# Kernel tuning notes

Hardware: AMD Instinct MI355X
Metric: run time of the kernel (lower is better)

The kernel has to match this reference:

```python
import jax, jax.numpy as jnp
import numpy as np

B, D, H, K, P = 16384, 64, 256, 8, 3  # batch, lattice dim, hidden, expressivity, num_pars


def setup_inputs() -> dict:
    key = jax.random.key(0)
    k0, k1, k2 = jax.random.split(key, 3)
    # U(1) angles in [0, 2*pi)
    z = jax.random.uniform(k0, (B, D), dtype=jnp.float32) * (2.0 * jnp.pi)
    # per-step conditioner MLP weights, padded to full input dim (causally masked in reference)
    W1 = jax.random.normal(k1, (D - 1, D, H), dtype=jnp.float32) * 0.05
    b1 = jnp.zeros((D - 1, H), dtype=jnp.float32)
    W2 = jax.random.normal(k2, (D - 1, H, P * K), dtype=jnp.float32) * 0.05
    b2 = jnp.zeros((D - 1, P * K), dtype=jnp.float32)
    return {"z": z, "W1": W1, "b1": b1, "W2": W2, "b2": b2}


def reference(z, W1, b1, W2, b2):
    # decode(): x[...,0]=0; for idx in 1..D-1:
    #   params = conditioner_idx(z[..., :idx]); x[..., idx], ld = diffeo(z[..., idx], *params)
    # All conditioners read only z, so steps are independent -> vectorize over steps.
    d = z.shape[-1]
    r = d - 1
    # mask[row, col] = col < row+1  (conditioner idx uses first idx inputs)
    mask = (jnp.arange(d)[None, :] < (jnp.arange(r) + 1)[:, None]).astype(z.dtype)  # [R, D]
    W1m = W1 * mask[:, :, None]                                   # causal zero-padding
    h = jax.nn.relu(jnp.einsum('bd,rdh->brh', z, W1m) + b1)       # [B, R, H]
    raw = jnp.einsum('brh,rhp->brp', h, W2) + b2                  # [B, R, 3K]
    a_u, b_u, r_u = jnp.split(raw, 3, axis=-1)                    # each [B, R, K]
    alpha = jnp.exp(a_u)
    beta = b_u
    rho = jax.nn.softmax(r_u, axis=-1)
    # NCP diffeomorphism on U(1): convex mixture of 2*atan(alpha*tan((z-pi)/2)+beta)+pi
    zi = z[:, 1:]                                                  # [B, R]
    t = jnp.tan((zi - jnp.pi) * 0.5)[..., None]                    # [B, R, 1]
    g = alpha * t + beta                                           # [B, R, K]
    x_tail = jnp.sum(rho * (2.0 * jnp.arctan(g) + jnp.pi), axis=-1)
    deriv = alpha * (1.0 + t * t) / (1.0 + g * g)                  # dh/dz per component
    ld = jnp.log(jnp.sum(rho * deriv, axis=-1))                    # [B, R]
    x = jnp.concatenate([jnp.zeros_like(z[:, :1]), x_tail], axis=-1)
    log_det = jnp.sum(ld, axis=-1)                                 # [B]
    return x, log_det
```

## Files before the change

kernel.cpp:

```cpp
#include <hip/hip_runtime.h>
#include <math.h>
#include <type_traits>

typedef __bf16 bf16x8 __attribute__((ext_vector_type(8)));
typedef float f32x4 __attribute__((ext_vector_type(4)));
typedef unsigned int u32x4 __attribute__((ext_vector_type(4)));

#define B_TOT 16384
#define D_TOT 64
#define R_TOT 63
#define H_TOT 256
#define PK_TOT 24
#define PI_F 3.14159265358979323846f

#define W2F_BASE_U32 516096u
#define WS_NEED 3096576u

#define MFMA16(a, b, c) __builtin_amdgcn_mfma_f32_16x16x32_bf16((a), (b), (c), 0, 0, 0)

__device__ __forceinline__ unsigned short bf16_rtne(float f) {
    unsigned u = __float_as_uint(f);
    unsigned rr = u + 0x7FFFu + ((u >> 16) & 1u);
    return (unsigned short)(rr >> 16);
}

__device__ __forceinline__ unsigned cvt_pk_bf16(float a, float b) {
    unsigned r;
    asm("v_cvt_pk_bf16_f32 %0, %1, %2" : "=v"(r) : "v"(a), "v"(b));
    return r;
}

__global__ void init_out_kernel(float* __restrict__ out) {
    int b = blockIdx.x * 256 + threadIdx.x;
    if (b < B_TOT) {
        out[(size_t)b * D_TOT] = 0.0f;
        out[(size_t)B_TOT * D_TOT + b] = 0.0f;
    }
}

__global__ void prep_weights(const float* __restrict__ W1,
                             const float* __restrict__ b1,
                             const float* __restrict__ W2,
                             unsigned int* __restrict__ wsf)
{
    int gid = blockIdx.x * 256 + threadIdx.x;
    if (gid >= 193536) return;
    float v[8];
    unsigned int* dst;
    if (gid < 129024) {
        int lane = gid & 63;
        int q = gid >> 6;
        int t = q & 1; int qq = q >> 1;
        int nt = qq & 15; int r = qq >> 4;
        int n  = (nt << 4) + (lane & 15);
        int kb = (t << 5) + ((lane >> 4) << 3);
        int bias_d = (r <= 30) ? 31 : 63;
        #pragma unroll
        for (int j = 0; j < 8; ++j) {
            int d = kb + j;
            v[j] = (d <= r) ? W1[(size_t)(r * 64 + d) * 256 + n]
                 : (d == bias_d ? b1[(size_t)r * 256 + n] : 0.0f);
        }
        dst = wsf + (size_t)q * 256 + ((unsigned)lane << 2);
    } else {
        int g2 = gid - 129024;
        int lane = g2 & 63;
        int q = g2 >> 6;
        int ks = q & 7; int qq = q >> 3;
        int nt = qq & 1; int r = qq >> 1;
        int n  = (nt << 4) + (lane & 15);
        int kb = (ks << 5) + ((lane >> 4) << 3);
        #pragma unroll
        for (int j = 0; j < 8; ++j) {
            int k = kb + j;
            v[j] = (n < PK_TOT) ? W2[(size_t)(r * 256 + k) * PK_TOT + n] : 0.0f;
        }
        dst = wsf + W2F_BASE_U32 + (size_t)q * 256 + ((unsigned)lane << 2);
    }
    unsigned hw[4];
    #pragma unroll
    for (int i = 0; i < 4; ++i)
        hw[i] = (unsigned)bf16_rtne(v[2 * i]) | ((unsigned)bf16_rtne(v[2 * i + 1]) << 16);
    *reinterpret_cast<u32x4*>(dst) = u32x4{hw[0], hw[1], hw[2], hw[3]};
}

__global__ __launch_bounds__(256, 4) void flow_mfma(
    const float* __restrict__ z, const unsigned int* __restrict__ wsf,
    const float* __restrict__ b2, float* __restrict__ out)
{
    const int y   = blockIdx.y;
    int r0, r1;
    if (y < 15)       { r0 = 2 * y;     r1 = 2 * y + 1; }
    else if (y == 15) { r0 = 30;        r1 = -1;        }
    else              { r0 = 2 * y - 1; r1 = 2 * y;     }
    const int bias_d = (y <= 15) ? 31 : 63;

    const int b0  = blockIdx.x << 6;
    const int tid = threadIdx.x;
    const int w   = tid >> 6;
    const int l   = tid & 63;
    const int l15 = l & 15, l4 = l >> 4, key = l & 7;

    __shared__ __align__(16) unsigned char sm[25088];
    float* tls = reinterpret_cast<float*>(sm + 24576);

    {
        const int m  = tid >> 2;
        const int dq = (tid & 3) << 4;
        const float* zp = z + (size_t)(b0 + m) * 64 + dq;
        const int mkey = m & 7;
        const int rel  = bias_d - dq;
        const int tel0 = (r0 + 1) - dq;
        const int tel1 = (r1 + 1) - dq;
        #pragma unroll
        for (int qq = 0; qq < 4; ++qq) {
            float4 val = *reinterpret_cast<const float4*>(zp + (qq << 2));
            int d0 = dq + (qq << 2);
            float vv[4] = {val.x, val.y, val.z, val.w};
            if ((tel0 >> 2) == qq) {
                float zi = vv[tel0 & 3];
                float s, c;
                __sincosf(zi * 0.5f, &s, &c);
                float t = -c * __builtin_amdgcn_rcpf(s);
                tls[m] = fminf(fmaxf(t, -1e8f), 1e8f);
            }
            if ((tel1 >> 2) == qq) {
                float zi = vv[tel1 & 3];
                float s, c;
                __sincosf(zi * 0.5f, &s, &c);
                float t = -c * __builtin_amdgcn_rcpf(s);
                tls[64 + m] = fminf(fmaxf(t, -1e8f), 1e8f);
            }
            if ((rel >> 2) == qq) vv[rel & 3] = 1.0f;
            uint2 hv;
            hv.x = cvt_pk_bf16(vv[0], vv[1]);
            hv.y = cvt_pk_bf16(vv[2], vv[3]);
            int off = (m << 7) + ((((d0 >> 3)) ^ mkey) << 4) + (((d0 >> 2) & 1) << 3);
            *reinterpret_cast<uint2*>(sm + off) = hv;
        }
    }
    __syncthreads();

    const int ej = tid & 7;
    float ld0 = 0.0f, ld1 = 0.0f;

    #pragma unroll 1
    for (int ri = 0; ri < 2; ++ri) {
        const int r = ri ? r1 : r0;
        if (r < 0) break;

        const unsigned int* w1b = wsf + (size_t)((r * 16 + (w << 2)) * 2) * 256 + (l << 2);
        const unsigned int* w2b = wsf + W2F_BASE_U32 + (size_t)(r * 16) * 256 + (l << 2);
        const float b2a = b2[(size_t)r * 24 + ej];
        const float b2b = b2[(size_t)r * 24 + 8 + ej];
        const float b2r = b2[(size_t)r * 24 + 16 + ej];

        #pragma unroll 1
        for (int mh = 0; mh < 2; ++mh) {
            f32x4 acc1[4][2];
            #pragma unroll
            for (int a = 0; a < 4; ++a)
                #pragma unroll
                for (int b = 0; b < 2; ++b) acc1[a][b] = f32x4{0.f, 0.f, 0.f, 0.f};

            auto run_gemm1 = [&](auto FULLC) {
                constexpr int NT = decltype(FULLC)::value ? 2 : 1;
                #pragma unroll
                for (int t = 0; t < NT; ++t) {
                    bf16x8 zf[2];
                    #pragma unroll
                    for (int mt = 0; mt < 2; ++mt) {
                        int m = (mh << 5) + (mt << 4) + l15;
                        int off = (m << 7) + ((((t << 2) + l4) ^ key) << 4);
                        zf[mt] = __builtin_bit_cast(bf16x8, *reinterpret_cast<u32x4*>(sm + off));
                    }
                    #pragma unroll
                    for (int ntl = 0; ntl < 4; ++ntl) {
                        bf16x8 af = __builtin_bit_cast(bf16x8,
                            *reinterpret_cast<const u32x4*>(w1b + (((ntl << 1) + t) << 8)));
                        #pragma unroll
                        for (int mt = 0; mt < 2; ++mt)
                            acc1[ntl][mt] = MFMA16(af, zf[mt], acc1[ntl][mt]);
                    }
                }
            };
            if (r >= 31) run_gemm1(std::true_type{});
            else         run_gemm1(std::false_type{});

            #pragma unroll
            for (int ntl = 0; ntl < 4; ++ntl) {
                #pragma unroll
                for (int mt = 0; mt < 2; ++mt) {
                    float v0 = fmaxf(acc1[ntl][mt][0], 0.0f);
                    float v1 = fmaxf(acc1[ntl][mt][1], 0.0f);
                    float v2 = fmaxf(acc1[ntl][mt][2], 0.0f);
                    float v3 = fmaxf(acc1[ntl][mt][3], 0.0f);
                    uint2 hv;
                    hv.x = cvt_pk_bf16(v0, v1);
                    hv.y = cvt_pk_bf16(v2, v3);
                    int mloc = (mt << 4) + l15;
                    int g    = (w << 3) + (ntl << 1) + (l4 >> 1);
                    int off  = 8192 + (mloc << 9)
                             + (((g & 24) | ((g ^ key) & 7)) << 4) + ((l4 & 1) << 3);
                    *reinterpret_cast<uint2*>(sm + off) = hv;
                }
            }
            __syncthreads();

            f32x4 acc2[2][2];
            #pragma unroll
            for (int a = 0; a < 2; ++a)
                #pragma unroll
                for (int b = 0; b < 2; ++b) acc2[a][b] = f32x4{0.f, 0.f, 0.f, 0.f};

            #pragma unroll
            for (int kk = 0; kk < 2; ++kk) {
                const int ks = (w << 1) + kk;
                bf16x8 wf[2];
                #pragma unroll
                for (int nt2 = 0; nt2 < 2; ++nt2)
                    wf[nt2] = __builtin_bit_cast(bf16x8,
                        *reinterpret_cast<const u32x4*>(w2b + (((nt2 << 3) + ks) << 8)));
                bf16x8 hfr[2];
                #pragma unroll
                for (int mt = 0; mt < 2; ++mt) {
                    int mloc = (mt << 4) + l15;
                    int g    = (ks << 2) + l4;
                    int off  = 8192 + (mloc << 9)
                             + (((g & 24) | ((g ^ key) & 7)) << 4);
                    hfr[mt] = __builtin_bit_cast(bf16x8, *reinterpret_cast<u32x4*>(sm + off));
                }
                #pragma unroll
                for (int nt2 = 0; nt2 < 2; ++nt2)
                    #pragma unroll
                    for (int mt = 0; mt < 2; ++mt)
                        acc2[nt2][mt] = MFMA16(wf[nt2], hfr[mt], acc2[nt2][mt]);
            }
            __syncthreads();

            #pragma unroll
            for (int nt2 = 0; nt2 < 2; ++nt2)
                #pragma unroll
                for (int mt = 0; mt < 2; ++mt) {
                    int row = (w << 5) + (mt << 4) + l15;
                    int off = 8192 + (row << 7) + ((((nt2 << 2) + l4) ^ key) << 4);
                    *reinterpret_cast<f32x4*>(sm + off) = acc2[nt2][mt];
                }
            __syncthreads();

            {
                const int mloc = tid >> 3;
                const int j    = ej;
                const int mk   = mloc & 7;
                float ra = b2a, rb = b2b, rr = b2r;
                #pragma unroll
                for (int w4 = 0; w4 < 4; ++w4) {
                    const int base = 8192 + (((w4 << 5) + mloc) << 7);
                    const int sub  = (j & 3) << 2;
                    ra += *reinterpret_cast<float*>(sm + base + ((((j) >> 2) ^ mk) << 4) + sub);
                    rb += *reinterpret_cast<float*>(sm + base + (((2 + (j >> 2)) ^ mk) << 4) + sub);
                    rr += *reinterpret_cast<float*>(sm + base + (((4 + (j >> 2)) ^ mk) << 4) + sub);
                }
                int gb = b0 + (mh << 5) + mloc;
                float t  = tls[(ri << 6) + (mh << 5) + mloc];
                float al = __expf(ra);
                float g  = fmaf(al, t, rb);
                float X  = 2.0f * atanf(g) + PI_F;
                float dv = al * fmaf(t, t, 1.0f) * __builtin_amdgcn_rcpf(fmaf(g, g, 1.0f));
                float mx = rr;
                mx = fmaxf(mx, __shfl_xor(mx, 1));
                mx = fmaxf(mx, __shfl_xor(mx, 2));
                mx = fmaxf(mx, __shfl_xor(mx, 4));
                float e = __expf(rr - mx);
                float se = e, sx = e * X, sd = e * dv;
                se += __shfl_xor(se, 1); se += __shfl_xor(se, 2); se += __shfl_xor(se, 4);
                sx += __shfl_xor(sx, 1); sx += __shfl_xor(sx, 2); sx += __shfl_xor(sx, 4);
                sd += __shfl_xor(sd, 1); sd += __shfl_xor(sd, 2); sd += __shfl_xor(sd, 4);
                if (j == 0) {
                    float rse = __builtin_amdgcn_rcpf(se);
                    out[(size_t)gb * D_TOT + r + 1] = sx * rse;
                    float ldv = __logf(sd * rse);
                    if (mh == 0) ld0 += ldv; else ld1 += ldv;
                }
            }
            __syncthreads();
        }
    }

    if (ej == 0) {
        const int mloc = tid >> 3;
        atomicAdd(&out[(size_t)B_TOT * D_TOT + b0 + mloc], ld0);
        atomicAdd(&out[(size_t)B_TOT * D_TOT + b0 + 32 + mloc], ld1);
    }
}

__global__ __launch_bounds__(256, 2) void flow_fp32(
    const float* __restrict__ z,  const float* __restrict__ W1,
    const float* __restrict__ b1, const float* __restrict__ W2,
    const float* __restrict__ b2, float* __restrict__ out)
{
    const int r   = blockIdx.y;
    const int b0  = blockIdx.x * 32;
    const int tid = threadIdx.x;

    __shared__ float smem[16384];
    float* z_t  = smem;
    float* h_s  = smem + 2048;
    float* w2t  = smem + 2048 + 8192;
    float* part = w2t;

    #pragma unroll
    for (int it = 0; it < 2; ++it) {
        int idx4 = it * 256 + tid;
        int brow = idx4 >> 4;
        int dq   = (idx4 & 15) << 2;
        float4 v = *reinterpret_cast<const float4*>(&z[(size_t)(b0 + brow) * D_TOT + dq]);
        z_t[(dq + 0) * 32 + brow] = v.x;
        z_t[(dq + 1) * 32 + brow] = v.y;
        z_t[(dq + 2) * 32 + brow] = v.z;
        z_t[(dq + 3) * 32 + brow] = v.w;
    }
    #pragma unroll
    for (int it = 0; it < 6; ++it) {
        int idx4 = it * 256 + tid;
        int k  = idx4 / 6;
        int pq = (idx4 - k * 6) << 2;
        float4 v = *reinterpret_cast<const float4*>(&W2[(size_t)(r * H_TOT + k) * PK_TOT + pq]);
        int gk = k >> 2, kq = k & 3;
        w2t[(pq + 0) * 256 + (((gk) ^ ((pq + 0) & 7)) << 2) + kq] = v.x;
        w2t[(pq + 1) * 256 + (((gk) ^ ((pq + 1) & 7)) << 2) + kq] = v.y;
        w2t[(pq + 2) * 256 + (((gk) ^ ((pq + 2) & 7)) << 2) + kq] = v.z;
        w2t[(pq + 3) * 256 + (((gk) ^ ((pq + 3) & 7)) << 2) + kq] = v.w;
    }
    __syncthreads();

    const int rg = tid & 15;
    const int cg = tid >> 4;
    float acc[2][16];
    #pragma unroll
    for (int j = 0; j < 2; ++j)
        #pragma unroll
        for (int i = 0; i < 16; ++i) acc[j][i] = 0.0f;

    const float* w1p = W1 + (size_t)(r * D_TOT) * H_TOT + (cg << 4);
    #pragma unroll 4
    for (int d = 0; d <= r; ++d) {
        float2 zv = *reinterpret_cast<const float2*>(&z_t[d * 32 + (rg << 1)]);
        const float* wrow = w1p + (size_t)d * H_TOT;
        float wv[16];
        *reinterpret_cast<float4*>(&wv[0])  = *reinterpret_cast<const float4*>(wrow + 0);
        *reinterpret_cast<float4*>(&wv[4])  = *reinterpret_cast<const float4*>(wrow + 4);
        *reinterpret_cast<float4*>(&wv[8])  = *reinterpret_cast<const float4*>(wrow + 8);
        *reinterpret_cast<float4*>(&wv[12]) = *reinterpret_cast<const float4*>(wrow + 12);
        #pragma unroll
        for (int i = 0; i < 16; ++i) {
            acc[0][i] = fmaf(zv.x, wv[i], acc[0][i]);
            acc[1][i] = fmaf(zv.y, wv[i], acc[1][i]);
        }
    }
    {
        const int key = (rg >> 1) & 7;
        #pragma unroll
        for (int gi = 0; gi < 4; ++gi) {
            float4 bv = *reinterpret_cast<const float4*>(&b1[(size_t)r * H_TOT + (cg << 4) + (gi << 2)]);
            #pragma unroll
            for (int j = 0; j < 2; ++j) {
                float4 v;
                v.x = fmaxf(acc[j][4 * gi + 0] + bv.x, 0.0f);
                v.y = fmaxf(acc[j][4 * gi + 1] + bv.y, 0.0f);
                v.z = fmaxf(acc[j][4 * gi + 2] + bv.z, 0.0f);
                v.w = fmaxf(acc[j][4 * gi + 3] + bv.w, 0.0f);
                int bb = (rg << 1) + j;
                int g  = ((cg << 2) + gi) ^ key;
                *reinterpret_cast<float4*>(&h_s[bb * 256 + (g << 2)]) = v;
            }
        }
    }
    __syncthreads();

    const int wv_ = tid >> 6;
    const int ln  = tid & 63;
    const int bq  = ln & 7;
    const int pg  = ln >> 3;
    float acc2[4][3];
    #pragma unroll
    for (int j = 0; j < 4; ++j)
        #pragma unroll
        for (int i = 0; i < 3; ++i) acc2[j][i] = 0.0f;

    #pragma unroll
    for (int c = 0; c < 8; ++c) {
        int k0  = (wv_ << 6) + (c << 3);
        int gk0 = k0 >> 2;
        float w2r[3][8], hr[4][8];
        #pragma unroll
        for (int i = 0; i < 3; ++i) {
            int p = 3 * pg + i, pk = p & 7;
            *reinterpret_cast<float4*>(&w2r[i][0]) =
                *reinterpret_cast<const float4*>(&w2t[p * 256 + (((gk0 + 0) ^ pk) << 2)]);
            *reinterpret_cast<float4*>(&w2r[i][4]) =
                *reinterpret_cast<const float4*>(&w2t[p * 256 + (((gk0 + 1) ^ pk) << 2)]);
        }
        #pragma unroll
        for (int j = 0; j < 4; ++j) {
            int bb = 4 * bq + j;
            *reinterpret_cast<float4*>(&hr[j][0]) =
                *reinterpret_cast<const float4*>(&h_s[bb * 256 + (((gk0 + 0) ^ bq) << 2)]);
            *reinterpret_cast<float4*>(&hr[j][4]) =
                *reinterpret_cast<const float4*>(&h_s[bb * 256 + (((gk0 + 1) ^ bq) << 2)]);
        }
        #pragma unroll
        for (int kk = 0; kk < 8; ++kk)
            #pragma unroll
            for (int j = 0; j < 4; ++j)
                #pragma unroll
                for (int i = 0; i < 3; ++i)
                    acc2[j][i] = fmaf(hr[j][kk], w2r[i][kk], acc2[j][i]);
    }
    __syncthreads();
    #pragma unroll
    for (int j = 0; j < 4; ++j)
        #pragma unroll
        for (int i = 0; i < 3; ++i)
            part[((wv_ << 5) + 4 * bq + j) * PK_TOT + 3 * pg + i] = acc2[j][i];
    __syncthreads();

    {
        const int eb = tid >> 3;
        const int ej = tid & 7;
        float rawa = b2[(size_t)r * PK_TOT + ej];
        float rawb = b2[(size_t)r * PK_TOT + 8 + ej];
        float rawr = b2[(size_t)r * PK_TOT + 16 + ej];
        #pragma unroll
        for (int w = 0; w < 4; ++w) {
            rawa += part[((w << 5) + eb) * PK_TOT + ej];
            rawb += part[((w << 5) + eb) * PK_TOT + 8 + ej];
            rawr += part[((w << 5) + eb) * PK_TOT + 16 + ej];
        }
        float zi = z_t[(r + 1) * 32 + eb];
        float t  = tanf((zi - PI_F) * 0.5f);
        float al = expf(rawa);
        float g  = fmaf(al, t, rawb);
        float X  = 2.0f * atanf(g) + PI_F;
        float dv = al * (1.0f + t * t) / (1.0f + g * g);
        float m = rawr;
        m = fmaxf(m, __shfl_xor(m, 1));
        m = fmaxf(m, __shfl_xor(m, 2));
        m = fmaxf(m, __shfl_xor(m, 4));
        float e  = expf(rawr - m);
        float se = e, sx = e * X, sd = e * dv;
        se += __shfl_xor(se, 1); se += __shfl_xor(se, 2); se += __shfl_xor(se, 4);
        sx += __shfl_xor(sx, 1); sx += __shfl_xor(sx, 2); sx += __shfl_xor(sx, 4);
        sd += __shfl_xor(sd, 1); sd += __shfl_xor(sd, 2); sd += __shfl_xor(sd, 4);
        if (ej == 0) {
            int gb = b0 + eb;
            out[(size_t)gb * D_TOT + (r + 1)] = sx / se;
            atomicAdd(&out[(size_t)B_TOT * D_TOT + gb], logf(sd / se));
        }
    }
}

extern "C" void kernel_launch(void* const* d_in, const int* in_sizes, int n_in,
                              void* d_out, int out_size, void* d_ws, size_t ws_size,
                              hipStream_t stream) {
    const float* z  = (const float*)d_in[0];
    const float* W1 = (const float*)d_in[1];
    const float* b1 = (const float*)d_in[2];
    const float* W2 = (const float*)d_in[3];
    const float* b2 = (const float*)d_in[4];
    float* out = (float*)d_out;

    init_out_kernel<<<dim3(B_TOT / 256), dim3(256), 0, stream>>>(out);
    if (ws_size >= (size_t)WS_NEED) {
        prep_weights<<<dim3(756), dim3(256), 0, stream>>>(W1, b1, W2, (unsigned int*)d_ws);
        flow_mfma<<<dim3(B_TOT / 64, 32), dim3(256), 0, stream>>>(
            z, (const unsigned int*)d_ws, b2, out);
    } else {
        flow_fp32<<<dim3(B_TOT / 32, R_TOT), dim3(256), 0, stream>>>(z, W1, b1, W2, b2, out);
    }
}
```

Baseline: 103.5 us.

## Repartition second GEMM by output tile per wave to drop split-K reduction

The second GEMM now gives each wave one (m-tile, n-tile) output and has it run all 8 K-steps, instead of each wave covering a K slice for every tile. This removes the split-K partial-sum store, one barrier, and the four-way reduction read in the epilogue. Results go to a separate shared region, which lets the trailing barrier be dropped, and launch bounds rise to 5 blocks per CU. The price is more shared memory per block and a longer serial MFMA chain per wave.

```diff
diff --git a/kernel.cpp b/kernel.cpp
--- a/kernel.cpp
+++ b/kernel.cpp
@@ -84,7 +84,7 @@
     *reinterpret_cast<u32x4*>(dst) = u32x4{hw[0], hw[1], hw[2], hw[3]};
 }
 
-__global__ __launch_bounds__(256, 4) void flow_mfma(
+__global__ __launch_bounds__(256, 5) void flow_mfma(
     const float* __restrict__ z, const unsigned int* __restrict__ wsf,
     const float* __restrict__ b2, float* __restrict__ out)
 {
@@ -100,8 +100,10 @@
     const int w   = tid >> 6;
     const int l   = tid & 63;
     const int l15 = l & 15, l4 = l >> 4, key = l & 7;
-
-    __shared__ __align__(16) unsigned char sm[25088];
+    const int mt  = w & 1;
+    const int nt2 = w >> 1;
+
+    __shared__ __align__(16) unsigned char sm[29184];
     float* tls = reinterpret_cast<float*>(sm + 24576);
 
     {
@@ -169,18 +171,18 @@
                 for (int t = 0; t < NT; ++t) {
                     bf16x8 zf[2];
                     #pragma unroll
-                    for (int mt = 0; mt < 2; ++mt) {
-                        int m = (mh << 5) + (mt << 4) + l15;
+                    for (int mtz = 0; mtz < 2; ++mtz) {
+                        int m = (mh << 5) + (mtz << 4) + l15;
                         int off = (m << 7) + ((((t << 2) + l4) ^ key) << 4);
-                        zf[mt] = __builtin_bit_cast(bf16x8, *reinterpret_cast<u32x4*>(sm + off));
+                        zf[mtz] = __builtin_bit_cast(bf16x8, *reinterpret_cast<u32x4*>(sm + off));
                     }
                     #pragma unroll
                     for (int ntl = 0; ntl < 4; ++ntl) {
                         bf16x8 af = __builtin_bit_cast(bf16x8,
                             *reinterpret_cast<const u32x4*>(w1b + (((ntl << 1) + t) << 8)));
                         #pragma unroll
-                        for (int mt = 0; mt < 2; ++mt)
-                            acc1[ntl][mt] = MFMA16(af, zf[mt], acc1[ntl][mt]);
+                        for (int mtz = 0; mtz < 2; ++mtz)
+                            acc1[ntl][mtz] = MFMA16(af, zf[mtz], acc1[ntl][mtz]);
                     }
                 }
             };
@@ -190,15 +192,15 @@
             #pragma unroll
             for (int ntl = 0; ntl < 4; ++ntl) {
                 #pragma unroll
-                for (int mt = 0; mt < 2; ++mt) {
-                    float v0 = fmaxf(acc1[ntl][mt][0], 0.0f);
-                    float v1 = fmaxf(acc1[ntl][mt][1], 0.0f);
-                    float v2 = fmaxf(acc1[ntl][mt][2], 0.0f);
-                    float v3 = fmaxf(acc1[ntl][mt][3], 0.0f);
+                for (int mtz = 0; mtz < 2; ++mtz) {
+                    float v0 = fmaxf(acc1[ntl][mtz][0], 0.0f);
+                    float v1 = fmaxf(acc1[ntl][mtz][1], 0.0f);
+                    float v2 = fmaxf(acc1[ntl][mtz][2], 0.0f);
+                    float v3 = fmaxf(acc1[ntl][mtz][3], 0.0f);
                     uint2 hv;
                     hv.x = cvt_pk_bf16(v0, v1);
                     hv.y = cvt_pk_bf16(v2, v3);
-                    int mloc = (mt << 4) + l15;
+                    int mloc = (mtz << 4) + l15;
                     int g    = (w << 3) + (ntl << 1) + (l4 >> 1);
                     int off  = 8192 + (mloc << 9)
                              + (((g & 24) | ((g ^ key) & 7)) << 4) + ((l4 & 1) << 3);
@@ -207,60 +209,32 @@
             }
             __syncthreads();
 
-            f32x4 acc2[2][2];
-            #pragma unroll
-            for (int a = 0; a < 2; ++a)
+            f32x4 acc2 = f32x4{0.f, 0.f, 0.f, 0.f};
+            {
+                const int mrow  = (mt << 4) + l15;
+                const int hbase = 8192 + (mrow << 9);
                 #pragma unroll
-                for (int b = 0; b < 2; ++b) acc2[a][b] = f32x4{0.f, 0.f, 0.f, 0.f};
-
-            #pragma unroll
-            for (int kk = 0; kk < 2; ++kk) {
-                const int ks = (w << 1) + kk;
-                bf16x8 wf[2];
-                #pragma unroll
-                for (int nt2 = 0; nt2 < 2; ++nt2)
-                    wf[nt2] = __builtin_bit_cast(bf16x8,
+                for (int ks = 0; ks < 8; ++ks) {
+                    bf16x8 wf = __builtin_bit_cast(bf16x8,
                         *reinterpret_cast<const u32x4*>(w2b + (((nt2 << 3) + ks) << 8)));
-                bf16x8 hfr[2];
-                #pragma unroll
-                for (int mt = 0; mt < 2; ++mt) {
-                    int mloc = (mt << 4) + l15;
-                    int g    = (ks << 2) + l4;
-                    int off  = 8192 + (mloc << 9)
-                             + (((g & 24) | ((g ^ key) & 7)) << 4);
-                    hfr[mt] = __builtin_bit_cast(bf16x8, *reinterpret_cast<u32x4*>(sm + off));
+                    int g = (ks << 2) + l4;
+                    bf16x8 hfr = __builtin_bit_cast(bf16x8,
+                        *reinterpret_cast<u32x4*>(sm + hbase + (((g & 24) | ((g ^ key) & 7)) << 4)));
+                    acc2 = MFMA16(wf, hfr, acc2);
                 }
-                #pragma unroll
-                for (int nt2 = 0; nt2 < 2; ++nt2)
-                    #pragma unroll
-                    for (int mt = 0; mt < 2; ++mt)
-                        acc2[nt2][mt] = MFMA16(wf[nt2], hfr[mt], acc2[nt2][mt]);
-            }
-            __syncthreads();
-
-            #pragma unroll
-            for (int nt2 = 0; nt2 < 2; ++nt2)
-                #pragma unroll
-                for (int mt = 0; mt < 2; ++mt) {
-                    int row = (w << 5) + (mt << 4) + l15;
-                    int off = 8192 + (row << 7) + ((((nt2 << 2) + l4) ^ key) << 4);
-                    *reinterpret_cast<f32x4*>(sm + off) = acc2[nt2][mt];
-                }
+                int gr = ((nt2 << 2) + l4) ^ (mrow & 7);
+                *reinterpret_cast<f32x4*>(sm + 25088 + (mrow << 7) + (gr << 4)) = acc2;
+            }
             __syncthreads();
 
             {
                 const int mloc = tid >> 3;
-                const int j    = ej;
                 const int mk   = mloc & 7;
-                float ra = b2a, rb = b2b, rr = b2r;
-                #pragma unroll
-                for (int w4 = 0; w4 < 4; ++w4) {
-                    const int base = 8192 + (((w4 << 5) + mloc) << 7);
-                    const int sub  = (j & 3) << 2;
-                    ra += *reinterpret_cast<float*>(sm + base + ((((j) >> 2) ^ mk) << 4) + sub);
-                    rb += *reinterpret_cast<float*>(sm + base + (((2 + (j >> 2)) ^ mk) << 4) + sub);
-                    rr += *reinterpret_cast<float*>(sm + base + (((4 + (j >> 2)) ^ mk) << 4) + sub);
-                }
+                const int base = 25088 + (mloc << 7);
+                const int sub  = (ej & 3) << 2;
+                float ra = b2a + *reinterpret_cast<float*>(sm + base + ((((ej >> 2)    ) ^ mk) << 4) + sub);
+                float rb = b2b + *reinterpret_cast<float*>(sm + base + (((2 + (ej >> 2)) ^ mk) << 4) + sub);
+                float rr = b2r + *reinterpret_cast<float*>(sm + base + (((4 + (ej >> 2)) ^ mk) << 4) + sub);
                 int gb = b0 + (mh << 5) + mloc;
                 float t  = tls[(ri << 6) + (mh << 5) + mloc];
                 float al = __expf(ra);
@@ -276,14 +250,13 @@
                 se += __shfl_xor(se, 1); se += __shfl_xor(se, 2); se += __shfl_xor(se, 4);
                 sx += __shfl_xor(sx, 1); sx += __shfl_xor(sx, 2); sx += __shfl_xor(sx, 4);
                 sd += __shfl_xor(sd, 1); sd += __shfl_xor(sd, 2); sd += __shfl_xor(sd, 4);
-                if (j == 0) {
+                if (ej == 0) {
                     float rse = __builtin_amdgcn_rcpf(se);
                     out[(size_t)gb * D_TOT + r + 1] = sx * rse;
                     float ldv = __logf(sd * rse);
                     if (mh == 0) ld0 += ldv; else ld1 += ldv;
                 }
             }
-            __syncthreads();
         }
     }
 
```

New measurement: 178.0 us. +72.0%, slower.
